# Performance work log

Measured on AMD Instinct MI355X. Metric: run time of the kernel, lower is better.

Reference implementation:

```python
import math
import jax, jax.numpy as jnp
import numpy as np

THETA = 2.0 ** 16
TWO_PI = 2.0 * math.pi


def _freqs(N):
    # quantize(arange(N), 2) = floor(t/2)*2 -> paired frequencies
    idx = jnp.floor(jnp.arange(N, dtype=jnp.float32) / 2.0) * 2.0
    return 1.0 / (THETA ** (idx / N)) / TWO_PI  # (N,)


def _rope(v, cos, sin):
    # rotate pairs: (-v_odd, v_even) interleaved back to original layout
    v_rot = jnp.stack((-v[..., 1::2], v[..., ::2]), axis=-1).reshape(v.shape)
    return v * cos + v_rot * sin


def setup_inputs() -> dict:
    key = jax.random.key(0)
    k1, k2 = jax.random.split(key)
    B, nh, T, N, D = 1, 4, 2048, 8192, 256
    Q = jax.random.normal(k1, (B, nh, T, N), dtype=jnp.float32) * 0.02
    V = jax.random.normal(k2, (B, 1, T, D), dtype=jnp.float32)
    return {"Q": Q, "V": V}


def reference(Q, V):
    # Q: (B, nh, T, N) sparse neuron space; V: (B, 1, T, D) embedding space; K is Q
    T, N = Q.shape[2], Q.shape[3]
    freqs = _freqs(N)
    phases = jnp.arange(T, dtype=jnp.float32)[:, None] * freqs[None, :]  # (T, N)
    ang = (phases % 1.0) * TWO_PI
    cos, sin = jnp.cos(ang), jnp.sin(ang)
    QR = _rope(Q, cos, sin)  # (B, nh, T, N)
    scores = jnp.einsum('bhtn,bhsn->bhts', QR, QR)  # (B, nh, T, T)
    causal = jnp.tril(jnp.ones((T, T), dtype=bool), k=-1)  # strictly lower
    scores = jnp.where(causal, scores, 0.0)
    # V broadcasts over heads: (B, nh, T, T) @ (B, 1, T, D) -> (B, nh, T, D)
    return jnp.matmul(scores, V)
```

## Files before the change

### kernel.cpp

```cpp
#include <hip/hip_runtime.h>

#define LDS_AS __attribute__((address_space(3)))
#define GLB_AS __attribute__((address_space(1)))

typedef __attribute__((ext_vector_type(8))) short bf16x8;
typedef __attribute__((ext_vector_type(4))) float f32x4;
typedef __attribute__((ext_vector_type(16))) float f32x16;

static constexpr int NH = 4;
static constexpr int T  = 2048;
static constexpr int N  = 8192;
static constexpr int D  = 256;

__device__ inline unsigned short f2bf(float f) {
    unsigned int u = __float_as_uint(f);
    u += 0x7FFFu + ((u >> 16) & 1u);
    return (unsigned short)(u >> 16);
}

__device__ inline void gl2lds16(const void* g, void* l) {
    __builtin_amdgcn_global_load_lds((GLB_AS void*)g, (LDS_AS void*)l, 16, 0, 0);
}

__global__ void rope_kernel(const float* __restrict__ Q, unsigned short* __restrict__ QR) {
    int g = blockIdx.x * 256 + threadIdx.x;
    int base = g << 2;
    int n = base & (N - 1);
    int t = (base >> 13) & (T - 1);
    const float4 q = *(const float4*)(Q + (size_t)base);
    float tf = (float)t;
    const float inv2pi = 0.15915494309189535f;
    float f0 = exp2f((float)n       * (-1.0f / 512.0f)) * inv2pi;
    float f1 = exp2f((float)(n + 2) * (-1.0f / 512.0f)) * inv2pi;
    float r0 = tf * f0; r0 -= floorf(r0);
    float r1 = tf * f1; r1 -= floorf(r1);
    float s0 = __builtin_amdgcn_sinf(r0), c0 = __builtin_amdgcn_cosf(r0);
    float s1 = __builtin_amdgcn_sinf(r1), c1 = __builtin_amdgcn_cosf(r1);
    ushort4 o;
    o.x = f2bf(q.x * c0 - q.y * s0);
    o.y = f2bf(q.y * c0 + q.x * s0);
    o.z = f2bf(q.z * c1 - q.w * s1);
    o.w = f2bf(q.w * c1 + q.z * s1);
    *(ushort4*)(QR + (size_t)base) = o;
}

__global__ void vt_kernel(const float* __restrict__ V, unsigned short* __restrict__ Vt) {
    __shared__ unsigned short tile[64 * 65];
    int tb = blockIdx.x >> 2, db = blockIdx.x & 3;
    int t0 = tb * 64, d0 = db * 64;
    int tid = threadIdx.x;
    #pragma unroll
    for (int r = 0; r < 16; r++) {
        int idx = tid + r * 256;
        int tl = idx >> 6, dl = idx & 63;
        tile[tl * 65 + dl] = f2bf(V[(size_t)(t0 + tl) * D + d0 + dl]);
    }
    __syncthreads();
    #pragma unroll
    for (int r = 0; r < 16; r++) {
        int idx = tid + r * 256;
        int dl = idx >> 6, tl = idx & 63;
        Vt[(size_t)(d0 + dl) * T + t0 + tl] = tile[tl * 65 + dl];
    }
}

__global__ __launch_bounds__(256, 2) void gemm1_kernel(const unsigned short* __restrict__ QR,
                                                       unsigned short* __restrict__ S, int KS) {
    __shared__ __align__(16) unsigned short As[3][4096];
    __shared__ __align__(16) unsigned short Bs[3][8192];

    int bx = blockIdx.x;
    int per_h = 72 * KS;
    int h = bx / per_h;
    int rem = bx % per_h;
    int task = rem / KS;
    int ksp = rem % KS;
    int bi = 0, cum = 0;
    for (; bi < 16; bi++) { int nb = (bi >> 1) + 1; if (cum + nb > task) break; cum += nb; }
    int bj = task - cum;

    const unsigned short* A = QR + (size_t)h * T * N + (size_t)bi * 128 * N;
    const unsigned short* B = QR + (size_t)h * T * N + (size_t)bj * 256 * N;

    int KN = N / KS;
    int k_begin = ksp * KN;
    int nit = KN / 32;

    int tid = threadIdx.x;
    int lane = tid & 63, wave = tid >> 6;
    int wm = wave >> 1, wn = wave & 1;

    int blk0 = wave;
    int rowA = ((blk0 >> 1) << 5) + (lane & 31);
    int kkA  = ((blk0 & 1) << 4) + ((lane >> 5) << 3);
    const unsigned short* Asrc = A + (size_t)rowA * N + kkA;
    const unsigned short* Bsrc = B + (size_t)rowA * N + kkA;

    f32x16 acc[2][4];
    #pragma unroll
    for (int i = 0; i < 2; i++)
        #pragma unroll
        for (int j = 0; j < 4; j++)
            #pragma unroll
            for (int r = 0; r < 16; r++) acc[i][j][r] = 0.0f;

    #pragma unroll
    for (int p = 0; p < 2; p++) {
        int k0 = k_begin + p * 32;
        gl2lds16(Asrc + k0,                   &As[p][tid * 8]);
        gl2lds16(Asrc + (size_t)64 * N + k0,  &As[p][2048 + tid * 8]);
        gl2lds16(Bsrc + k0,                   &Bs[p][tid * 8]);
        gl2lds16(Bsrc + (size_t)64 * N + k0,  &Bs[p][2048 + tid * 8]);
        gl2lds16(Bsrc + (size_t)128 * N + k0, &Bs[p][4096 + tid * 8]);
        gl2lds16(Bsrc + (size_t)192 * N + k0, &Bs[p][6144 + tid * 8]);
    }

    int cur = 0, nxt2 = 2;
    for (int it = 0; it < nit; it++) {
        if (it + 1 < nit) {
            asm volatile("s_waitcnt vmcnt(6)" ::: "memory");
        } else {
            asm volatile("s_waitcnt vmcnt(0)" ::: "memory");
        }
        __builtin_amdgcn_s_barrier();
        __builtin_amdgcn_sched_barrier(0);

        bf16x8 a2[2][2], b2[4][2];
        #pragma unroll
        for (int i = 0; i < 2; i++)
            #pragma unroll
            for (int kk = 0; kk < 2; kk++)
                a2[i][kk] = *(const bf16x8*)&As[cur][(((wm * 2 + i) * 2 + kk) << 9) + lane * 8];
        #pragma unroll
        for (int j = 0; j < 4; j++)
            #pragma unroll
            for (int kk = 0; kk < 2; kk++)
                b2[j][kk] = *(const bf16x8*)&Bs[cur][(((wn * 4 + j) * 2 + kk) << 9) + lane * 8];

        if (it + 2 < nit) {
            int k0 = k_begin + (it + 2) * 32;
            gl2lds16(Asrc + k0,                   &As[nxt2][tid * 8]);
            gl2lds16(Asrc + (size_t)64 * N + k0,  &As[nxt2][2048 + tid * 8]);
            gl2lds16(Bsrc + k0,                   &Bs[nxt2][tid * 8]);
            gl2lds16(Bsrc + (size_t)64 * N + k0,  &Bs[nxt2][2048 + tid * 8]);
            gl2lds16(Bsrc + (size_t)128 * N + k0, &Bs[nxt2][4096 + tid * 8]);
            gl2lds16(Bsrc + (size_t)192 * N + k0, &Bs[nxt2][6144 + tid * 8]);
        }

        __builtin_amdgcn_s_setprio(1);
        #pragma unroll
        for (int kk = 0; kk < 2; kk++)
            #pragma unroll
            for (int j = 0; j < 4; j++)
                #pragma unroll
                for (int i = 0; i < 2; i++)
                    acc[i][j] = __builtin_amdgcn_mfma_f32_32x32x16_bf16(a2[i][kk], b2[j][kk],
                                                                        acc[i][j], 0, 0, 0);
        __builtin_amdgcn_s_setprio(0);

        cur  = (cur  == 2) ? 0 : cur  + 1;
        nxt2 = (nxt2 == 2) ? 0 : nxt2 + 1;
    }

    unsigned short* Sh = S + (size_t)ksp * NH * T * T + (size_t)h * T * T;
    int col = lane & 31;
    int rbase = (lane >> 5) * 4;
    #pragma unroll
    for (int i = 0; i < 2; i++) {
        #pragma unroll
        for (int j = 0; j < 4; j++) {
            int s_g = bj * 256 + wn * 128 + j * 32 + col;
            #pragma unroll
            for (int reg = 0; reg < 16; reg++) {
                int t_g = bi * 128 + wm * 64 + i * 32 + (reg & 3) + 8 * (reg >> 2) + rbase;
                float v = (s_g < t_g) ? acc[i][j][reg] : 0.0f;
                Sh[(size_t)t_g * T + s_g] = f2bf(v);
            }
        }
    }
}

__global__ __launch_bounds__(256) void gemm2_kernel(const unsigned short* __restrict__ S,
                                                    const unsigned short* __restrict__ Vt,
                                                    float* __restrict__ out, int KS) {
    __shared__ __align__(16) unsigned short As[2][128 * 32];
    __shared__ __align__(16) unsigned short Bs[2][128 * 32];

    int bx = blockIdx.x;
    int per_h = 2 * 72;
    int h = bx / per_h;
    int rem = bx % per_h;
    int dblk = rem / 72;
    int tc = rem % 72;
    int bi = 0, cum = 0;
    for (; bi < 16; bi++) { int nc = (bi + 2) >> 1; if (cum + nc > tc) break; cum += nc; }
    int c = tc - cum;

    int kend = (bi + 1) * 128;
    int cstart = c * 256;
    int clen = min(256, kend - cstart);
    int cpk = clen >> 5;
    int ls = (KS == 4) ? 2 : (KS == 2) ? 1 : 0;
    int nit = cpk << ls;

    const unsigned short* Sh = S + (size_t)h * T * T + (size_t)bi * 128 * T + cstart;
    const size_t sstride = (size_t)NH * T * T;
    const unsigned short* B = Vt + (size_t)dblk * 128 * T + cstart;

    int tid = threadIdx.x;
    int lane = tid & 63, wave = tid >> 6;
    int wm = wave >> 1, wn = wave & 1;
    int quad = lane >> 4, l16 = lane & 15;
    int srow = tid >> 2;
    int scol = (tid & 3) * 8;

    f32x4 acc[4][4];
    #pragma unroll
    for (int i = 0; i < 4; i++)
        #pragma unroll
        for (int j = 0; j < 4; j++)
            #pragma unroll
            for (int r = 0; r < 4; r++) acc[i][j][r] = 0.0f;

    gl2lds16(Sh + (size_t)srow * T + scol,        &As[0][srow * 32 + scol]);
    gl2lds16(Sh + (size_t)(srow + 64) * T + scol, &As[0][(srow + 64) * 32 + scol]);
    gl2lds16(B + (size_t)srow * T + scol,         &Bs[0][srow * 32 + scol]);
    gl2lds16(B + (size_t)(srow + 64) * T + scol,  &Bs[0][(srow + 64) * 32 + scol]);

    bf16x8 b[4];
    for (int i = 0; i < nit; i++) {
        int k0i = i >> ls;
        int ks  = i & (KS - 1);
        __syncthreads();
        if (i + 1 < nit) {
            int ksn = (i + 1) & (KS - 1);
            int k0n = (i + 1) >> ls;
            const unsigned short* An = Sh + (size_t)ksn * sstride + k0n * 32;
            int pan = (i + 1) & 1;
            gl2lds16(An + (size_t)srow * T + scol,        &As[pan][srow * 32 + scol]);
            gl2lds16(An + (size_t)(srow + 64) * T + scol, &As[pan][(srow + 64) * 32 + scol]);
            if (ksn == 0) {
                const unsigned short* Bn = B + k0n * 32;
                int pbn = k0n & 1;
                gl2lds16(Bn + (size_t)srow * T + scol,        &Bs[pbn][srow * 32 + scol]);
                gl2lds16(Bn + (size_t)(srow + 64) * T + scol, &Bs[pbn][(srow + 64) * 32 + scol]);
            }
        }

        int pa = i & 1, pb = k0i & 1;
        if (ks == 0) {
            #pragma unroll
            for (int j = 0; j < 4; j++)
                b[j] = *(const bf16x8*)&Bs[pb][(wn * 64 + j * 16 + l16) * 32 + quad * 8];
        }
        bf16x8 a[4];
        #pragma unroll
        for (int ii = 0; ii < 4; ii++)
            a[ii] = *(const bf16x8*)&As[pa][(wm * 64 + ii * 16 + l16) * 32 + quad * 8];
        #pragma unroll
        for (int ii = 0; ii < 4; ii++)
            #pragma unroll
            for (int j = 0; j < 4; j++)
                acc[ii][j] = __builtin_amdgcn_mfma_f32_16x16x32_bf16(a[ii], b[j], acc[ii][j], 0, 0, 0);
    }

    float* oh = out + (size_t)h * T * D;
    #pragma unroll
    for (int i = 0; i < 4; i++) {
        int t_base = bi * 128 + wm * 64 + i * 16 + quad * 4;
        #pragma unroll
        for (int j = 0; j < 4; j++) {
            int d_g = dblk * 128 + wn * 64 + j * 16 + l16;
            #pragma unroll
            for (int r = 0; r < 4; r++) {
                int t_g = t_base + r;
                atomicAdd(&oh[(size_t)t_g * D + d_g], acc[i][j][r]);
            }
        }
    }
}

extern "C" void kernel_launch(void* const* d_in, const int* in_sizes, int n_in,
                              void* d_out, int out_size, void* d_ws, size_t ws_size,
                              hipStream_t stream) {
    const float* Q = (const float*)d_in[0];
    const float* V = (const float*)d_in[1];
    float* out = (float*)d_out;

    const size_t qr_elems = (size_t)NH * T * N;
    const size_t vt_elems = (size_t)D * T;
    const size_t s_elems  = (size_t)NH * T * T;

    int KS = 1;
    for (int cand : {4, 2, 1}) {
        if (ws_size >= (qr_elems + vt_elems + (size_t)cand * s_elems) * sizeof(unsigned short)) {
            KS = cand; break;
        }
    }
    if (ws_size < (qr_elems + vt_elems + (size_t)KS * s_elems) * sizeof(unsigned short)) return;

    unsigned short* QR = (unsigned short*)d_ws;
    unsigned short* Vt = QR + qr_elems;
    unsigned short* S  = Vt + vt_elems;

    rope_kernel<<<(NH * T * N / 4) / 256, 256, 0, stream>>>(Q, QR);
    vt_kernel<<<(T / 64) * (D / 64), 256, 0, stream>>>(V, Vt);
    gemm1_kernel<<<NH * 72 * KS, 256, 0, stream>>>(QR, S, KS);
    hipMemsetAsync(d_out, 0, (size_t)out_size * sizeof(float), stream);
    gemm2_kernel<<<NH * 2 * 72, 256, 0, stream>>>(S, Vt, out, KS);
}
```

Measured before the change: 658.9 us.

## Swizzle LDS tile layout and triple-buffer gemm2 with single barrier pipeline

In the score GEMM, global-to-LDS loads now use a row-major 32-wide tile with an XOR swizzle on 16-byte chunks, and the fragment reads apply the same swizzle. The goal is fewer LDS bank conflicts and more contiguous global rows. The second GEMM moves from double to triple buffering with a prefetch distance of two, uses a vmcnt wait plus a single barrier, and adopts the same swizzle. It also reloads V fragments on every split-k step instead of reusing them, adds setprio, and sets launch_bounds to 2 blocks per SM. The costs are more LDS and redundant B loads when KS is greater than 1.

After: 588.9 us. -10.6%, faster.

```diff
diff --git a/kernel.cpp b/kernel.cpp
--- a/kernel.cpp
+++ b/kernel.cpp
@@ -90,11 +90,11 @@
     int lane = tid & 63, wave = tid >> 6;
     int wm = wave >> 1, wn = wave & 1;
 
-    int blk0 = wave;
-    int rowA = ((blk0 >> 1) << 5) + (lane & 31);
-    int kkA  = ((blk0 & 1) << 4) + ((lane >> 5) << 3);
-    const unsigned short* Asrc = A + (size_t)rowA * N + kkA;
-    const unsigned short* Bsrc = B + (size_t)rowA * N + kkA;
+    int srow = tid >> 2;
+    int q = tid & 3;
+    int scol_sw = (q ^ ((srow >> 1) & 3)) * 8;
+    const unsigned short* Asrc = A + (size_t)srow * N + scol_sw;
+    const unsigned short* Bsrc = B + (size_t)srow * N + scol_sw;
 
     f32x16 acc[2][4];
     #pragma unroll
@@ -115,6 +115,8 @@
         gl2lds16(Bsrc + (size_t)192 * N + k0, &Bs[p][6144 + tid * 8]);
     }
 
+    int l31 = lane & 31, hi = lane >> 5, fl = (lane >> 1) & 3;
+
     int cur = 0, nxt2 = 2;
     for (int it = 0; it < nit; it++) {
         if (it + 1 < nit) {
@@ -130,12 +132,14 @@
         for (int i = 0; i < 2; i++)
             #pragma unroll
             for (int kk = 0; kk < 2; kk++)
-                a2[i][kk] = *(const bf16x8*)&As[cur][(((wm * 2 + i) * 2 + kk) << 9) + lane * 8];
+                a2[i][kk] = *(const bf16x8*)&As[cur][(wm * 64 + i * 32 + l31) * 32
+                                                     + ((kk * 2 + hi) ^ fl) * 8];
         #pragma unroll
         for (int j = 0; j < 4; j++)
             #pragma unroll
             for (int kk = 0; kk < 2; kk++)
-                b2[j][kk] = *(const bf16x8*)&Bs[cur][(((wn * 4 + j) * 2 + kk) << 9) + lane * 8];
+                b2[j][kk] = *(const bf16x8*)&Bs[cur][(wn * 128 + j * 32 + l31) * 32
+                                                     + ((kk * 2 + hi) ^ fl) * 8];
 
         if (it + 2 < nit) {
             int k0 = k_begin + (it + 2) * 32;
@@ -180,11 +184,11 @@
     }
 }
 
-__global__ __launch_bounds__(256) void gemm2_kernel(const unsigned short* __restrict__ S,
-                                                    const unsigned short* __restrict__ Vt,
-                                                    float* __restrict__ out, int KS) {
-    __shared__ __align__(16) unsigned short As[2][128 * 32];
-    __shared__ __align__(16) unsigned short Bs[2][128 * 32];
+__global__ __launch_bounds__(256, 2) void gemm2_kernel(const unsigned short* __restrict__ S,
+                                                       const unsigned short* __restrict__ Vt,
+                                                       float* __restrict__ out, int KS) {
+    __shared__ __align__(16) unsigned short As[3][4096];
+    __shared__ __align__(16) unsigned short Bs[3][4096];
 
     int bx = blockIdx.x;
     int per_h = 2 * 72;
@@ -211,8 +215,10 @@
     int lane = tid & 63, wave = tid >> 6;
     int wm = wave >> 1, wn = wave & 1;
     int quad = lane >> 4, l16 = lane & 15;
+
     int srow = tid >> 2;
-    int scol = (tid & 3) * 8;
+    int q = tid & 3;
+    int scol_sw = (q ^ ((srow >> 1) & 3)) * 8;
 
     f32x4 acc[4][4];
     #pragma unroll
@@ -222,46 +228,57 @@
             #pragma unroll
             for (int r = 0; r < 4; r++) acc[i][j][r] = 0.0f;
 
-    gl2lds16(Sh + (size_t)srow * T + scol,        &As[0][srow * 32 + scol]);
-    gl2lds16(Sh + (size_t)(srow + 64) * T + scol, &As[0][(srow + 64) * 32 + scol]);
-    gl2lds16(B + (size_t)srow * T + scol,         &Bs[0][srow * 32 + scol]);
-    gl2lds16(B + (size_t)(srow + 64) * T + scol,  &Bs[0][(srow + 64) * 32 + scol]);
-
-    bf16x8 b[4];
+    #pragma unroll
+    for (int p = 0; p < 2; p++) {
+        int ks0 = p & (KS - 1);
+        int k00 = (p >> ls) * 32;
+        const unsigned short* An = Sh + (size_t)ks0 * sstride + k00;
+        const unsigned short* Bn = B + k00;
+        gl2lds16(An + (size_t)srow * T + scol_sw,        &As[p][tid * 8]);
+        gl2lds16(An + (size_t)(srow + 64) * T + scol_sw, &As[p][2048 + tid * 8]);
+        gl2lds16(Bn + (size_t)srow * T + scol_sw,        &Bs[p][tid * 8]);
+        gl2lds16(Bn + (size_t)(srow + 64) * T + scol_sw, &Bs[p][2048 + tid * 8]);
+    }
+
+    int fl16 = (l16 >> 1) & 3;
+    int cur = 0, nxt2 = 2;
     for (int i = 0; i < nit; i++) {
-        int k0i = i >> ls;
-        int ks  = i & (KS - 1);
-        __syncthreads();
         if (i + 1 < nit) {
-            int ksn = (i + 1) & (KS - 1);
-            int k0n = (i + 1) >> ls;
-            const unsigned short* An = Sh + (size_t)ksn * sstride + k0n * 32;
-            int pan = (i + 1) & 1;
-            gl2lds16(An + (size_t)srow * T + scol,        &As[pan][srow * 32 + scol]);
-            gl2lds16(An + (size_t)(srow + 64) * T + scol, &As[pan][(srow + 64) * 32 + scol]);
-            if (ksn == 0) {
-                const unsigned short* Bn = B + k0n * 32;
-                int pbn = k0n & 1;
-                gl2lds16(Bn + (size_t)srow * T + scol,        &Bs[pbn][srow * 32 + scol]);
-                gl2lds16(Bn + (size_t)(srow + 64) * T + scol, &Bs[pbn][(srow + 64) * 32 + scol]);
-            }
-        }
-
-        int pa = i & 1, pb = k0i & 1;
-        if (ks == 0) {
-            #pragma unroll
-            for (int j = 0; j < 4; j++)
-                b[j] = *(const bf16x8*)&Bs[pb][(wn * 64 + j * 16 + l16) * 32 + quad * 8];
-        }
-        bf16x8 a[4];
-        #pragma unroll
-        for (int ii = 0; ii < 4; ii++)
-            a[ii] = *(const bf16x8*)&As[pa][(wm * 64 + ii * 16 + l16) * 32 + quad * 8];
+            asm volatile("s_waitcnt vmcnt(4)" ::: "memory");
+        } else {
+            asm volatile("s_waitcnt vmcnt(0)" ::: "memory");
+        }
+        __builtin_amdgcn_s_barrier();
+        __builtin_amdgcn_sched_barrier(0);
+
+        bf16x8 a[4], b[4];
+        #pragma unroll
+        for (int ii = 0; ii < 4; ii++) {
+            a[ii] = *(const bf16x8*)&As[cur][(wm * 64 + ii * 16 + l16) * 32 + (quad ^ fl16) * 8];
+            b[ii] = *(const bf16x8*)&Bs[cur][(wn * 64 + ii * 16 + l16) * 32 + (quad ^ fl16) * 8];
+        }
+
+        if (i + 2 < nit) {
+            int ksn = (i + 2) & (KS - 1);
+            int k0n = ((i + 2) >> ls) * 32;
+            const unsigned short* An = Sh + (size_t)ksn * sstride + k0n;
+            const unsigned short* Bn = B + k0n;
+            gl2lds16(An + (size_t)srow * T + scol_sw,        &As[nxt2][tid * 8]);
+            gl2lds16(An + (size_t)(srow + 64) * T + scol_sw, &As[nxt2][2048 + tid * 8]);
+            gl2lds16(Bn + (size_t)srow * T + scol_sw,        &Bs[nxt2][tid * 8]);
+            gl2lds16(Bn + (size_t)(srow + 64) * T + scol_sw, &Bs[nxt2][2048 + tid * 8]);
+        }
+
+        __builtin_amdgcn_s_setprio(1);
         #pragma unroll
         for (int ii = 0; ii < 4; ii++)
             #pragma unroll
             for (int j = 0; j < 4; j++)
                 acc[ii][j] = __builtin_amdgcn_mfma_f32_16x16x32_bf16(a[ii], b[j], acc[ii][j], 0, 0, 0);
+        __builtin_amdgcn_s_setprio(0);
+
+        cur  = (cur  == 2) ? 0 : cur  + 1;
+        nxt2 = (nxt2 == 2) ? 0 : nxt2 + 1;
     }
 
     float* oh = out + (size_t)h * T * D;
```
